# Performance work log

Measured on AMD Instinct MI355X. Metric: run time of the kernel, lower is better.

The kernel has to match this reference:

```python
import jax, jax.numpy as jnp
import numpy as np


def setup_inputs() -> dict:
    key = jax.random.key(0)
    k1, k2, k3 = jax.random.split(key, 3)
    B, C, L = 4, 64, 4096
    proj_query = jax.random.normal(k1, (B, C, L), dtype=jnp.float32)
    proj_key = jax.random.normal(k2, (B, C, L), dtype=jnp.float32)
    proj_val = jax.random.normal(k3, (B, C, L), dtype=jnp.float32)
    padding_mask = jnp.ones((B, 1, L), dtype=jnp.float32)
    return {
        "proj_query": proj_query,
        "proj_key": proj_key,
        "proj_val": proj_val,
        "padding_mask": padding_mask,
    }


def reference(proj_query, proj_key, proj_val, padding_mask):
    # proj_query/key/val: [B, C, L]; padding_mask: [B, 1, L]
    B, C, L1 = proj_query.shape
    scale = 1.0 / np.sqrt(C).astype(np.float32)
    # energy[b, lq, lk] = sum_c q[b,c,lq] * k[b,c,lk]
    energy = jnp.einsum("bcq,bck->bqk", proj_query, proj_key)
    attention = energy * scale + jnp.log(padding_mask + 1e-6)  # mask broadcasts over lq
    attention = jax.nn.softmax(attention, axis=-1) * padding_mask
    attention_t = jnp.transpose(attention, (0, 2, 1))  # [B, lk, lq]
    # out[b, c, lq] = sum_lk v[b,c,lk] * attention_t[b,lk,lq]
    out = jnp.einsum("bck,bkq->bcq", proj_val, attention_t)
    return out, attention_t
```

## Files before the change

kernel.cpp:

```cpp
#include <hip/hip_runtime.h>
#include <stdint.h>

#define BB 4
#define CCH 64
#define LLEN 4096
#define QS2 0.18033688011112042f
#define TQ 64
#define TK 64
#define NCHUNK 8
#define TPC 8
#define NTB 256
#define TQE 128
#define NTE 512
#define NCHE 4
#define TPE 16

typedef __bf16 bf16;
typedef bf16 bf16x4 __attribute__((ext_vector_type(4)));
typedef bf16 bf16x8 __attribute__((ext_vector_type(8)));
typedef float f32x4 __attribute__((ext_vector_type(4)));

#define EXP2F(x) __builtin_amdgcn_exp2f(x)
#define LOG2F(x) __builtin_amdgcn_logf(x)

__device__ __forceinline__ int swz(int row, int col) {
    return row * 64 + (col ^ ((row & 7) << 3));
}

__device__ __forceinline__ void g2l16(const void* g, void* l) {
    __builtin_amdgcn_global_load_lds(
        (const __attribute__((address_space(1))) void*)g,
        (__attribute__((address_space(3))) void*)l, 16, 0, 0);
}

#define WAITVM0 asm volatile("s_waitcnt vmcnt(0)" ::: "memory")
#define WAITVM16 asm volatile("s_waitcnt vmcnt(16)" ::: "memory")
#define WAITLGKM0 asm volatile("s_waitcnt lgkmcnt(0)" ::: "memory")
#define BAR() __builtin_amdgcn_s_barrier()
#define PRIO(n) __builtin_amdgcn_s_setprio(n)

__device__ __forceinline__ void stage_rows(const bf16* src, bf16* dst, int w, int l) {
#pragma unroll
    for (int i = 0; i < 2; ++i) {
        int ci = w * 2 + i;
        g2l16(src + ci * 512 + l * 8, dst + ci * 512);
    }
}
__device__ __forceinline__ void stage_tile8(const bf16* src, bf16* dst, int w, int l) {
    g2l16(src + w * 512 + l * 8, dst + w * 512);
}

__global__ __launch_bounds__(NTB) void prep_all(
    const float* __restrict__ qg, const float* __restrict__ kg,
    const float* __restrict__ vg, const float* __restrict__ mg,
    bf16* __restrict__ qT, bf16* __restrict__ kT,
    bf16* __restrict__ vF, float* __restrict__ wS, float* __restrict__ wE)
{
    const int tid = threadIdx.x;
    if (blockIdx.x < 512) {
        __shared__ float t[64][65];
        const int isK = blockIdx.x >> 8;
        const int idx = blockIdx.x & 255;
        const int b = idx >> 6;
        const int lt = idx & 63;
        const float* src = (isK ? kg : qg) + (size_t)b * CCH * LLEN + lt * 64;
        bf16* dst = (isK ? kT : qT) + ((size_t)b * LLEN + lt * 64) * 64;

        int c = tid >> 2, x0 = (tid & 3) * 16;
#pragma unroll
        for (int j = 0; j < 4; ++j) {
            float4 f = *(const float4*)&src[(size_t)c * LLEN + x0 + j * 4];
            t[c][x0 + j * 4 + 0] = f.x;
            t[c][x0 + j * 4 + 1] = f.y;
            t[c][x0 + j * 4 + 2] = f.z;
            t[c][x0 + j * 4 + 3] = f.w;
        }
        __syncthreads();
        int lk = tid >> 2;
        int g0 = (tid & 3) * 2;
#pragma unroll
        for (int gi = 0; gi < 2; ++gi) {
            int gg = g0 + gi;
            bf16x8 v;
#pragma unroll
            for (int j = 0; j < 8; ++j) v[j] = (bf16)t[gg * 8 + j][lk];
            *(bf16x8*)&dst[lk * 64 + ((gg ^ (lk & 7)) * 8)] = v;
        }
    } else if (blockIdx.x < 768) {
        const int row = blockIdx.x - 512;
        const int b = row >> 6;
        const int c = row & 63;
        const int mt = c >> 4, cl = c & 15;
        const size_t base = (size_t)row * LLEN;
        const int x0 = tid * 16;
        const int tile = x0 >> 6;
        float f[16];
#pragma unroll
        for (int j = 0; j < 4; ++j) {
            float4 v4 = *(const float4*)&vg[base + x0 + j * 4];
            f[j * 4 + 0] = v4.x; f[j * 4 + 1] = v4.y;
            f[j * 4 + 2] = v4.z; f[j * 4 + 3] = v4.w;
        }
        bf16* vFb = vF + (size_t)(b * 64 + tile) * 4096;
#pragma unroll
        for (int k2 = 0; k2 < 4; ++k2) {
            int rem = (x0 & 63) + 4 * k2;
            int s = rem >> 5, hl = (rem >> 4) & 1, g = (rem >> 2) & 3;
            bf16x4 hv = {(bf16)f[4 * k2 + 0], (bf16)f[4 * k2 + 1],
                         (bf16)f[4 * k2 + 2], (bf16)f[4 * k2 + 3]};
            *(bf16x4*)&vFb[(size_t)(((s * 4 + mt) * 64 + 16 * g + cl) * 8 + hl * 4)] = hv;
        }
    } else {
        const int b = blockIdx.x - 768;
        int x0 = tid * 16;
#pragma unroll
        for (int j = 0; j < 16; ++j) {
            float m = mg[(size_t)b * LLEN + x0 + j];
            float w = m + 1e-6f;
            wS[(size_t)b * LLEN + x0 + j] = LOG2F(w);
            wE[(size_t)b * LLEN + x0 + j] = LOG2F(w * m);
        }
    }
}

__global__ __launch_bounds__(NTB) void attn_stats(
    const bf16* __restrict__ qT, const bf16* __restrict__ kT,
    const float* __restrict__ wS, float* __restrict__ sums,
    float* __restrict__ outp)
{
    __shared__ __align__(16) bf16 kbuf[2][TK * CCH];
    __shared__ __align__(16) float wbuf[2][TK];
    __shared__ float red[4][TQ];

    const int tid = threadIdx.x;
    const int l = tid & 63;
    const int w = tid >> 6;
    const int g = l >> 4;
    const int cl = l & 15;

    const int idx = blockIdx.x;
    const int chunk = idx & 7;
    const int lqt = (idx >> 3) & 63;
    const int b = idx >> 9;
    const int lq0 = lqt * TQ;
    const size_t bL = (size_t)b * LLEN;

    {
        size_t o = ((size_t)idx * NTB + tid) * 2;
        *(float2*)&outp[o] = make_float2(0.f, 0.f);
    }

    stage_rows(qT + (bL + lq0) * 64, kbuf[1], w, l);
    stage_rows(kT + (bL + chunk * 512) * 64, kbuf[0], w, l);
    if (w == 0 && l < 16) g2l16(wS + bL + chunk * 512 + l * 4, wbuf[0]);
    WAITVM0;
    BAR();
    bf16x8 qf[4][2];
#pragma unroll
    for (int strip = 0; strip < 4; ++strip) {
        qf[strip][0] = *(const bf16x8*)&kbuf[1][swz(strip * 16 + cl, 8 * g)];
        qf[strip][1] = *(const bf16x8*)&kbuf[1][swz(strip * 16 + cl, 32 + 8 * g)];
    }
    WAITLGKM0;
    BAR();

    float sacc[4] = {0.f, 0.f, 0.f, 0.f};
#pragma unroll
    for (int it = 0; it < TPC; ++it) {
        const int kcur = it & 1;
        const int lk0 = chunk * 512 + it * 64;

        if (it < TPC - 1) {
            stage_rows(kT + (bL + lk0 + 64) * 64, kbuf[kcur ^ 1], w, l);
            if (w == 0 && l < 16) g2l16(wS + bL + lk0 + 64 + l * 4, wbuf[kcur ^ 1]);
        }

        bf16x8 kf0 = *(const bf16x8*)&kbuf[kcur][swz(16 * w + cl, 8 * g)];
        bf16x8 kf1 = *(const bf16x8*)&kbuf[kcur][swz(16 * w + cl, 32 + 8 * g)];
        float4 wv = *(const float4*)&wbuf[kcur][16 * w + 4 * g];

        PRIO(1);
#pragma unroll
        for (int strip = 0; strip < 4; ++strip) {
            f32x4 e = (f32x4){0.f, 0.f, 0.f, 0.f};
            e = __builtin_amdgcn_mfma_f32_16x16x32_bf16(kf0, qf[strip][0], e, 0, 0, 0);
            e = __builtin_amdgcn_mfma_f32_16x16x32_bf16(kf1, qf[strip][1], e, 0, 0, 0);
            sacc[strip] += EXP2F(fmaf(e[0], QS2, wv.x));
            sacc[strip] += EXP2F(fmaf(e[1], QS2, wv.y));
            sacc[strip] += EXP2F(fmaf(e[2], QS2, wv.z));
            sacc[strip] += EXP2F(fmaf(e[3], QS2, wv.w));
        }
        PRIO(0);

        if (it < TPC - 1) {
            WAITVM0;
            WAITLGKM0;
            BAR();
        }
    }

#pragma unroll
    for (int strip = 0; strip < 4; ++strip) {
        sacc[strip] += __shfl_xor(sacc[strip], 16);
        sacc[strip] += __shfl_xor(sacc[strip], 32);
    }
    if (l < 16) {
#pragma unroll
        for (int strip = 0; strip < 4; ++strip) red[w][strip * 16 + l] = sacc[strip];
    }
    __syncthreads();
    if (tid < TQ) {
        float s = red[0][tid] + red[1][tid] + red[2][tid] + red[3][tid];
        sums[(bL + lq0 + tid) * NCHUNK + chunk] = s;
    }
}

__global__ __launch_bounds__(NTE, 4) void attn_emit(
    const bf16* __restrict__ qT, const bf16* __restrict__ kT,
    const bf16* __restrict__ vF, const float* __restrict__ wE,
    const float* __restrict__ sums, float* __restrict__ outp,
    float* __restrict__ attnT)
{
    __shared__ __align__(16) bf16 kbuf[2][TK * CCH];
    __shared__ __align__(16) bf16 vbuf[2][TK * CCH];
    __shared__ __align__(16) float wbuf[2][TK];

    const int tid = threadIdx.x;
    const int l = tid & 63;
    const int w = tid >> 6;
    const int strip = w * 16;
    const int g = l >> 4;
    const int cl = l & 15;

    const int idx = blockIdx.x;
    const int chunk = idx & (NCHE - 1);
    const int lqt = (idx >> 2) & 31;
    const int b = idx >> 7;
    const int lq0 = lqt * TQE;
    const size_t bL = (size_t)b * LLEN;
    const size_t obase = (size_t)b * CCH * LLEN;
    bf16* kflat = &kbuf[0][0];

    stage_rows(qT + (bL + lq0) * 64, kflat, w, l);
    float ls2;
    {
        const float4* sp = (const float4*)&sums[(bL + lq0 + strip + cl) * NCHUNK];
        float4 a = sp[0], c4 = sp[1];
        float ssum = ((a.x + a.y) + (a.z + a.w)) + ((c4.x + c4.y) + (c4.z + c4.w));
        ls2 = -LOG2F(ssum);
    }
    WAITVM0;
    BAR();
    bf16x8 qf0 = *(const bf16x8*)&kflat[swz(strip + cl, 8 * g)];
    bf16x8 qf1 = *(const bf16x8*)&kflat[swz(strip + cl, 32 + 8 * g)];
    WAITLGKM0;
    BAR();

    {
        const int lk0 = chunk * (TPE * TK);
        stage_tile8(kT + (bL + lk0) * 64, kbuf[0], w, l);
        stage_tile8(vF + (size_t)(b * 64 + (lk0 >> 6)) * 4096, vbuf[0], w, l);
        if (w == 0 && l < 16) g2l16(wE + bL + lk0 + l * 4, wbuf[0]);
    }
    WAITVM0;
    BAR();

    f32x4 o4[4];
#pragma unroll
    for (int t = 0; t < 4; ++t) o4[t] = (f32x4){0.f, 0.f, 0.f, 0.f};

#pragma unroll
    for (int it = 0; it < TPE; ++it) {
        const int cur = it & 1;
        const int lk0 = chunk * (TPE * TK) + it * 64;

        if (it < TPE - 1) {
            stage_tile8(kT + (bL + lk0 + 64) * 64, kbuf[cur ^ 1], w, l);
            stage_tile8(vF + (size_t)(b * 64 + (lk0 >> 6) + 1) * 4096, vbuf[cur ^ 1], w, l);
            if (w == 0 && l < 16) g2l16(wE + bL + lk0 + 64 + l * 4, wbuf[cur ^ 1]);
        }

        f32x4 e4[4];
#pragma unroll
        for (int t = 0; t < 4; ++t) e4[t] = (f32x4){0.f, 0.f, 0.f, 0.f};
        PRIO(1);
#pragma unroll
        for (int t = 0; t < 4; ++t) {
            bf16x8 kf0 = *(const bf16x8*)&kbuf[cur][swz(16 * t + cl, 8 * g)];
            e4[t] = __builtin_amdgcn_mfma_f32_16x16x32_bf16(kf0, qf0, e4[t], 0, 0, 0);
            bf16x8 kf1 = *(const bf16x8*)&kbuf[cur][swz(16 * t + cl, 32 + 8 * g)];
            e4[t] = __builtin_amdgcn_mfma_f32_16x16x32_bf16(kf1, qf1, e4[t], 0, 0, 0);
        }
        PRIO(0);

        float p[4][4];
#pragma unroll
        for (int t = 0; t < 4; ++t) {
            float4 wv = *(const float4*)&wbuf[cur][16 * t + 4 * g];
            p[t][0] = EXP2F(fmaf(e4[t][0], QS2, ls2 + wv.x));
            p[t][1] = EXP2F(fmaf(e4[t][1], QS2, ls2 + wv.y));
            p[t][2] = EXP2F(fmaf(e4[t][2], QS2, ls2 + wv.z));
            p[t][3] = EXP2F(fmaf(e4[t][3], QS2, ls2 + wv.w));
        }

        bf16x8 pb[2];
#pragma unroll
        for (int s = 0; s < 2; ++s)
#pragma unroll
            for (int j = 0; j < 8; ++j)
                pb[s][j] = (bf16)p[2 * s + (j >> 2)][j & 3];
        PRIO(1);
#pragma unroll
        for (int s = 0; s < 2; ++s) {
            bf16x8 vf4[4];
#pragma unroll
            for (int mt = 0; mt < 4; ++mt)
                vf4[mt] = *(const bf16x8*)&vbuf[cur][((s * 4 + mt) * 64 + l) * 8];
#pragma unroll
            for (int mt = 0; mt < 4; ++mt)
                o4[mt] = __builtin_amdgcn_mfma_f32_16x16x32_bf16(
                    vf4[mt], pb[s], o4[mt], 0, 0, 0);
        }
        PRIO(0);

#pragma unroll
        for (int t = 0; t < 4; ++t)
#pragma unroll
            for (int r = 0; r < 4; ++r) {
                int lkg = lk0 + 16 * t + 4 * g + r;
                attnT[(bL + lkg) * LLEN + lq0 + strip + cl] = p[t][r];
            }

        if (it < TPE - 1) {
            WAITVM16;
            WAITLGKM0;
            BAR();
        }
    }

#pragma unroll
    for (int mt = 0; mt < 4; ++mt)
#pragma unroll
        for (int r = 0; r < 4; ++r) {
            int c = 16 * mt + 4 * g + r;
            atomicAdd(&outp[obase + (size_t)c * LLEN + lq0 + strip + cl], o4[mt][r]);
        }
}

extern "C" void kernel_launch(void* const* d_in, const int* in_sizes, int n_in,
                              void* d_out, int out_size, void* d_ws, size_t ws_size,
                              hipStream_t stream) {
    const float* qg = (const float*)d_in[0];
    const float* kg = (const float*)d_in[1];
    const float* vg = (const float*)d_in[2];
    const float* mg = (const float*)d_in[3];
    float* outp = (float*)d_out;
    float* attnT = outp + (size_t)BB * CCH * LLEN;

    char* ws = (char*)d_ws;
    bf16* qT = (bf16*)ws;
    bf16* kT = (bf16*)(ws + (2u << 20));
    bf16* vF = (bf16*)(ws + (4u << 20));
    float* wS = (float*)(ws + (6u << 20));
    float* wE = (float*)(ws + (6u << 20) + (64u << 10));
    float* sums = (float*)(ws + (6u << 20) + (128u << 10));

    prep_all<<<772, NTB, 0, stream>>>(qg, kg, vg, mg, qT, kT, vF, wS, wE);
    attn_stats<<<BB * (LLEN / TQ) * NCHUNK, NTB, 0, stream>>>(qT, kT, wS, sums, outp);
    attn_emit<<<BB * (LLEN / TQE) * NCHE, NTE, 0, stream>>>(qT, kT, vF, wE, sums, outp, attnT);
}
```

Baseline: 92.67 us.

## Enlarge stats kernel query tile to 128 with 512 threads, fewer key chunks

Restructures the softmax-statistics kernel so each block handles 128 queries with 8 waves, two halves sharing each staged key tile, over 4 chunks of 16 key tiles instead of 8 chunks of 8. This halves the number of blocks and the key-tile reloads per query, and shortens the partial-sum vector the emit kernel reads. In exchange, each block is larger, the pipeline per block is longer, and fewer blocks are available for occupancy.

```diff
diff --git a/kernel.cpp b/kernel.cpp
--- a/kernel.cpp
+++ b/kernel.cpp
@@ -5,11 +5,12 @@
 #define CCH 64
 #define LLEN 4096
 #define QS2 0.18033688011112042f
-#define TQ 64
 #define TK 64
-#define NCHUNK 8
-#define TPC 8
 #define NTB 256
+#define TQS 128
+#define NTS 512
+#define NCHS 4
+#define TPS 16
 #define TQE 128
 #define NTE 512
 #define NCHE 4
@@ -123,76 +124,83 @@
     }
 }
 
-__global__ __launch_bounds__(NTB) void attn_stats(
+__global__ __launch_bounds__(NTS) void attn_stats(
     const bf16* __restrict__ qT, const bf16* __restrict__ kT,
     const float* __restrict__ wS, float* __restrict__ sums,
     float* __restrict__ outp)
 {
     __shared__ __align__(16) bf16 kbuf[2][TK * CCH];
     __shared__ __align__(16) float wbuf[2][TK];
-    __shared__ float red[4][TQ];
+    __shared__ float red[4][TQS];
 
     const int tid = threadIdx.x;
     const int l = tid & 63;
     const int w = tid >> 6;
+    const int sl = w & 3;
+    const int h = w >> 2;
     const int g = l >> 4;
     const int cl = l & 15;
 
     const int idx = blockIdx.x;
-    const int chunk = idx & 7;
-    const int lqt = (idx >> 3) & 63;
-    const int b = idx >> 9;
-    const int lq0 = lqt * TQ;
+    const int chunk = idx & (NCHS - 1);
+    const int lqt = (idx >> 2) & 31;
+    const int b = idx >> 7;
+    const int lq0 = lqt * TQS;
     const size_t bL = (size_t)b * LLEN;
+    bf16* kflat = &kbuf[0][0];
 
     {
-        size_t o = ((size_t)idx * NTB + tid) * 2;
-        *(float2*)&outp[o] = make_float2(0.f, 0.f);
-    }
-
-    stage_rows(qT + (bL + lq0) * 64, kbuf[1], w, l);
-    stage_rows(kT + (bL + chunk * 512) * 64, kbuf[0], w, l);
-    if (w == 0 && l < 16) g2l16(wS + bL + chunk * 512 + l * 4, wbuf[0]);
+        size_t o = ((size_t)idx * NTS + tid) * 4;
+        *(float4*)&outp[o] = make_float4(0.f, 0.f, 0.f, 0.f);
+    }
+
+    stage_rows(qT + (bL + lq0) * 64, kflat, w, l);
     WAITVM0;
     BAR();
     bf16x8 qf[4][2];
 #pragma unroll
-    for (int strip = 0; strip < 4; ++strip) {
-        qf[strip][0] = *(const bf16x8*)&kbuf[1][swz(strip * 16 + cl, 8 * g)];
-        qf[strip][1] = *(const bf16x8*)&kbuf[1][swz(strip * 16 + cl, 32 + 8 * g)];
+    for (int st = 0; st < 4; ++st) {
+        int row = h * 64 + st * 16 + cl;
+        qf[st][0] = *(const bf16x8*)&kflat[swz(row, 8 * g)];
+        qf[st][1] = *(const bf16x8*)&kflat[swz(row, 32 + 8 * g)];
     }
     WAITLGKM0;
     BAR();
 
+    const int lkbase = chunk * (TPS * TK);
+    stage_tile8(kT + (bL + lkbase) * 64, kbuf[0], w, l);
+    if (w == 0 && l < 16) g2l16(wS + bL + lkbase + l * 4, wbuf[0]);
+    WAITVM0;
+    BAR();
+
     float sacc[4] = {0.f, 0.f, 0.f, 0.f};
 #pragma unroll
-    for (int it = 0; it < TPC; ++it) {
-        const int kcur = it & 1;
-        const int lk0 = chunk * 512 + it * 64;
-
-        if (it < TPC - 1) {
-            stage_rows(kT + (bL + lk0 + 64) * 64, kbuf[kcur ^ 1], w, l);
-            if (w == 0 && l < 16) g2l16(wS + bL + lk0 + 64 + l * 4, wbuf[kcur ^ 1]);
-        }
-
-        bf16x8 kf0 = *(const bf16x8*)&kbuf[kcur][swz(16 * w + cl, 8 * g)];
-        bf16x8 kf1 = *(const bf16x8*)&kbuf[kcur][swz(16 * w + cl, 32 + 8 * g)];
-        float4 wv = *(const float4*)&wbuf[kcur][16 * w + 4 * g];
+    for (int it = 0; it < TPS; ++it) {
+        const int cur = it & 1;
+
+        if (it < TPS - 1) {
+            stage_tile8(kT + (bL + lkbase + (it + 1) * 64) * 64, kbuf[cur ^ 1], w, l);
+            if (w == 0 && l < 16) g2l16(wS + bL + lkbase + (it + 1) * 64 + l * 4, wbuf[cur ^ 1]);
+        }
+
+        bf16x8 kf0 = *(const bf16x8*)&kbuf[cur][swz(16 * sl + cl, 8 * g)];
+        bf16x8 kf1 = *(const bf16x8*)&kbuf[cur][swz(16 * sl + cl, 32 + 8 * g)];
+        float4 wv = *(const float4*)&wbuf[cur][16 * sl + 4 * g];
 
         PRIO(1);
 #pragma unroll
-        for (int strip = 0; strip < 4; ++strip) {
+        for (int st = 0; st < 4; ++st) {
             f32x4 e = (f32x4){0.f, 0.f, 0.f, 0.f};
-            e = __builtin_amdgcn_mfma_f32_16x16x32_bf16(kf0, qf[strip][0], e, 0, 0, 0);
-            e = __builtin_amdgcn_mfma_f32_16x16x32_bf16(kf1, qf[strip][1], e, 0, 0, 0);
-            sacc[strip] += EXP2F(fmaf(e[0], QS2, wv.x));
-            sacc[strip] += EXP2F(fmaf(e[1], QS2, wv.y));
-            sacc[strip] += EXP2F(fmaf(e[2], QS2, wv.z));
-            sacc[strip] += EXP2F(fmaf(e[3], QS2, wv.w));
+            e = __builtin_amdgcn_mfma_f32_16x16x32_bf16(kf0, qf[st][0], e, 0, 0, 0);
+            e = __builtin_amdgcn_mfma_f32_16x16x32_bf16(kf1, qf[st][1], e, 0, 0, 0);
+            sacc[st] += EXP2F(fmaf(e[0], QS2, wv.x));
+            sacc[st] += EXP2F(fmaf(e[1], QS2, wv.y));
+            sacc[st] += EXP2F(fmaf(e[2], QS2, wv.z));
+            sacc[st] += EXP2F(fmaf(e[3], QS2, wv.w));
         }
         PRIO(0);
 
-        if (it < TPC - 1) {
+        if (it < TPS - 1) {
             WAITVM0;
             WAITLGKM0;
             BAR();
@@ -200,18 +208,18 @@
     }
 
 #pragma unroll
-    for (int strip = 0; strip < 4; ++strip) {
-        sacc[strip] += __shfl_xor(sacc[strip], 16);
-        sacc[strip] += __shfl_xor(sacc[strip], 32);
+    for (int st = 0; st < 4; ++st) {
+        sacc[st] += __shfl_xor(sacc[st], 16);
+        sacc[st] += __shfl_xor(sacc[st], 32);
     }
     if (l < 16) {
 #pragma unroll
-        for (int strip = 0; strip < 4; ++strip) red[w][strip * 16 + l] = sacc[strip];
+        for (int st = 0; st < 4; ++st) red[sl][h * 64 + st * 16 + l] = sacc[st];
     }
     __syncthreads();
-    if (tid < TQ) {
-        float s = red[0][tid] + red[1][tid] + red[2][tid] + red[3][tid];
-        sums[(bL + lq0 + tid) * NCHUNK + chunk] = s;
+    if (tid < TQS) {
+        float s = (red[0][tid] + red[1][tid]) + (red[2][tid] + red[3][tid]);
+        sums[(bL + lq0 + tid) * NCHS + chunk] = s;
     }
 }
 
@@ -244,9 +252,8 @@
     stage_rows(qT + (bL + lq0) * 64, kflat, w, l);
     float ls2;
     {
-        const float4* sp = (const float4*)&sums[(bL + lq0 + strip + cl) * NCHUNK];
-        float4 a = sp[0], c4 = sp[1];
-        float ssum = ((a.x + a.y) + (a.z + a.w)) + ((c4.x + c4.y) + (c4.z + c4.w));
+        float4 a = *(const float4*)&sums[(bL + lq0 + strip + cl) * NCHS];
+        float ssum = (a.x + a.y) + (a.z + a.w);
         ls2 = -LOG2F(ssum);
     }
     WAITVM0;
@@ -366,6 +373,6 @@
     float* sums = (float*)(ws + (6u << 20) + (128u << 10));
 
     prep_all<<<772, NTB, 0, stream>>>(qg, kg, vg, mg, qT, kT, vF, wS, wE);
-    attn_stats<<<BB * (LLEN / TQ) * NCHUNK, NTB, 0, stream>>>(qT, kT, wS, sums, outp);
+    attn_stats<<<BB * (LLEN / TQS) * NCHS, NTS, 0, stream>>>(qT, kT, wS, sums, outp);
     attn_emit<<<BB * (LLEN / TQE) * NCHE, NTE, 0, stream>>>(qT, kT, vF, wE, sums, outp, attnT);
 }
```

After: 115.4 us. 1.25x slower.
